# Kernel tuning notes

Measured on AMD Instinct MI355X. Metric: run time of the kernel, lower is better.

## Reference

```python
import jax, jax.numpy as jnp
import numpy as np


def setup_inputs() -> dict:
    key = jax.random.key(0)
    k = jax.random.split(key, 6)
    B = 65536
    x = jax.random.normal(k[0], (B, 784), dtype=jnp.float32)
    conv_w = jax.random.normal(k[1], (3, 3), dtype=jnp.float32)
    # torch Linear: weight [out,in], bias [out]; uniform(-1/sqrt(in),1/sqrt(in)) init approximated
    fc1_w = jax.random.uniform(k[2], (128, 26 * 26), dtype=jnp.float32, minval=-1, maxval=1) / jnp.sqrt(676.0)
    fc1_b = jax.random.uniform(k[3], (128,), dtype=jnp.float32, minval=-1, maxval=1) / jnp.sqrt(676.0)
    fc2_w = jax.random.uniform(k[4], (10, 128), dtype=jnp.float32, minval=-1, maxval=1) / jnp.sqrt(128.0)
    fc2_b = jax.random.uniform(k[5], (10,), dtype=jnp.float32, minval=-1, maxval=1) / jnp.sqrt(128.0)
    return {"x": x, "conv_w": conv_w, "fc1_w": fc1_w, "fc1_b": fc1_b, "fc2_w": fc2_w, "fc2_b": fc2_b}


def _forward(x, conv_w, fc1_w, fc1_b, fc2_w, fc2_b):
    B = x.shape[0]
    img = x.reshape(B, 1, 28, 28)  # NCHW, single channel
    kern = conv_w.reshape(1, 1, 3, 3)  # OIHW
    # valid 3x3 cross-correlation -> (B,1,26,26), same math as the nested-loop Convolve
    conv = jax.lax.conv_general_dilated(
        img, kern, window_strides=(1, 1), padding="VALID",
        dimension_numbers=("NCHW", "OIHW", "NCHW"))
    h = conv.reshape(B, 26 * 26)
    h = jax.nn.relu(h @ fc1_w.T + fc1_b)
    return h @ fc2_w.T + fc2_b  # (B,10)


def reference(x, conv_w, fc1_w, fc1_b, fc2_w, fc2_b):
    return _forward(x, conv_w, fc1_w, fc1_b, fc2_w, fc2_b)
```

## Files before the change

kernel.cpp:

```cpp
#include <hip/hip_runtime.h>
#include <hip/hip_bf16.h>

typedef float  f32x4  __attribute__((ext_vector_type(4)));
typedef short  short8 __attribute__((ext_vector_type(8)));

#define NKT   25
#define BM    64
#define AB    4096
#define BB    8192
#define BOFFS (3 * AB)
#define POOLB (3 * AB + 3 * BB)

static __device__ __forceinline__ unsigned short f2bf(float f) {
    unsigned int u = __float_as_uint(f);
    unsigned int r = (u + 0x7fffu + ((u >> 16) & 1u)) >> 16;
    return (unsigned short)r;
}
static __device__ __forceinline__ float bf2f(unsigned short h) {
    return __uint_as_float(((unsigned int)h) << 16);
}
static __device__ __forceinline__ uint2 pack4(f32x4 v) {
    __hip_bfloat162 p0 = __float22bfloat162_rn(make_float2(v[0], v[1]));
    __hip_bfloat162 p1 = __float22bfloat162_rn(make_float2(v[2], v[3]));
    uint2 r;
    r.x = *reinterpret_cast<unsigned int*>(&p0);
    r.y = *reinterpret_cast<unsigned int*>(&p1);
    return r;
}

__global__ __launch_bounds__(256) void weff_prep(
    const float* __restrict__ fc1_w,
    const float* __restrict__ conv_w,
    const float* __restrict__ fc2_w,
    unsigned short* __restrict__ ws)
{
    int idx = blockIdx.x * 256 + threadIdx.x;
    if (idx >= 128 * 800) return;
    if (idx < 1280) ws[102400 + idx] = f2bf(fc2_w[idx]);
    int o = idx / 800, p = idx - o * 800;
    float s = 0.f;
    if (p < 784) {
        int y = p / 28, xx = p - y * 28;
        #pragma unroll
        for (int dr = 0; dr < 3; ++dr) {
            int r = y - dr;
            if (r < 0 || r > 25) continue;
            #pragma unroll
            for (int dc = 0; dc < 3; ++dc) {
                int c = xx - dc;
                if (c < 0 || c > 25) continue;
                s += fc1_w[o * 676 + r * 26 + c] * conv_w[dr * 3 + dc];
            }
        }
    }
    int kt = p >> 5, kk = p & 31;
    ws[kt * 4096 + (kk >> 3) * 1024 + o * 8 + (kk & 7)] = f2bf(s);
}

__global__ __launch_bounds__(512, 8) void fused_fwd(
    const float* __restrict__ x,
    const unsigned short* __restrict__ weff4,
    const float* __restrict__ fc1_b,
    const float* __restrict__ fc2_b,
    float* __restrict__ out,
    int B)
{
    __shared__ __align__(16) char pool[POOLB];

    const int tid  = threadIdx.x;
    const int lane = tid & 63;
    const int wid  = tid >> 6;
    const int wr   = wid >> 1;
    const int wc   = wid & 1;
    const int r16  = lane & 15;
    const int kc   = lane >> 4;
    const int m0   = blockIdx.x * BM;
    const unsigned short* fc2wb = weff4 + 102400;

    const int sr = tid >> 3;
    const int g  = tid & 7;
    int grow = m0 + sr; if (grow >= B) grow = B - 1;
    const float* xr = x + (size_t)grow * 784;
    const int awb = (g >> 1) * 1024 + sr * 16 + (g & 1) * 8;

    f32x4 av[4];

#define LD_A(s_, kt_) do {                                                    \
        int k_ = (kt_) * 32 + g * 4; if (k_ > 780) k_ = 0;                    \
        av[s_] = *reinterpret_cast<const f32x4*>(xr + k_);                    \
    } while (0)

#define WR_A(s_, bi_) do {                                                    \
        uint2 q_ = pack4(av[s_]);                                             \
        *reinterpret_cast<uint2*>(pool + (bi_) * AB + awb) = q_;              \
    } while (0)

#define GL_B(bi_, kt_) __builtin_amdgcn_global_load_lds(                      \
        (const __attribute__((address_space(1))) void*)                      \
            (weff4 + (size_t)(kt_) * 4096 + tid * 8),                         \
        (__attribute__((address_space(3))) void*)                            \
            (pool + BOFFS + (bi_) * BB + tid * 16), 16, 0, 0)

    const int aoff = kc * 1024 + (wr * 16 + r16) * 16;
    const int boff = BOFFS + kc * 2048 + (wc * 64 + r16) * 16;

    f32x4 acc[4];
    #pragma unroll
    for (int j = 0; j < 4; ++j) acc[j] = (f32x4)(0.f);

    asm volatile("s_waitcnt vmcnt(0)" ::: "memory");

    GL_B(0, 0); GL_B(1, 1);
    LD_A(0, 0); LD_A(1, 1); LD_A(2, 2);
    WR_A(0, 0);

    #pragma unroll
    for (int i = 0; i < NKT; ++i) {
        asm volatile("s_waitcnt vmcnt(3) lgkmcnt(0)" ::: "memory");
        __builtin_amdgcn_s_barrier();
        __builtin_amdgcn_sched_barrier(0);

        const char* pa = pool + (i % 3) * AB;
        const char* pb = pool + (i % 3) * BB;
        short8 a0 = *reinterpret_cast<const short8*>(pa + aoff);
        short8 b0 = *reinterpret_cast<const short8*>(pb + boff);
        short8 b1 = *reinterpret_cast<const short8*>(pb + boff + 256);
        short8 b2 = *reinterpret_cast<const short8*>(pb + boff + 512);
        short8 b3 = *reinterpret_cast<const short8*>(pb + boff + 768);

        const int kb = (i + 2 <= 24) ? (i + 2) : 24;
        const int ka = (i + 3 <= 24) ? (i + 3) : 24;
        GL_B((i + 2) % 3, kb);
        LD_A((i + 3) % 4, ka);
        WR_A((i + 1) % 4, (i + 1) % 3);

        acc[0] = __builtin_amdgcn_mfma_f32_16x16x32_bf16(a0, b0, acc[0], 0, 0, 0);
        acc[1] = __builtin_amdgcn_mfma_f32_16x16x32_bf16(a0, b1, acc[1], 0, 0, 0);
        acc[2] = __builtin_amdgcn_mfma_f32_16x16x32_bf16(a0, b2, acc[2], 0, 0, 0);
        acc[3] = __builtin_amdgcn_mfma_f32_16x16x32_bf16(a0, b3, acc[3], 0, 0, 0);
    }
#undef LD_A
#undef WR_A
#undef GL_B

    asm volatile("s_waitcnt vmcnt(0) lgkmcnt(0)" ::: "memory");
    __builtin_amdgcn_s_barrier();
    __builtin_amdgcn_sched_barrier(0);

    unsigned short (*Hs)[136] = (unsigned short (*)[136])pool;
    #pragma unroll
    for (int j = 0; j < 4; ++j) {
        int ncol = wc * 64 + j * 16 + r16;
        float bias = fc1_b[ncol];
        #pragma unroll
        for (int r = 0; r < 4; ++r) {
            int mrow = wr * 16 + kc * 4 + r;
            float h = acc[j][r] + bias;
            Hs[mrow][ncol] = f2bf(h > 0.f ? h : 0.f);
        }
    }
    __syncthreads();

    #pragma unroll
    for (int it = 0; it < 2; ++it) {
        int idx = it * 512 + tid;
        if (idx < BM * 10) {
            int row = idx / 10, j = idx - row * 10;
            if ((m0 + row) < B) {
                float sum = fc2_b[j];
                const unsigned short* wrow = fc2wb + j * 128;
                #pragma unroll
                for (int n8 = 0; n8 < 16; ++n8) {
                    short8 h = *reinterpret_cast<const short8*>(&Hs[row][n8 * 8]);
                    short8 w = *reinterpret_cast<const short8*>(wrow + n8 * 8);
                    #pragma unroll
                    for (int k2 = 0; k2 < 8; ++k2)
                        sum += bf2f(((unsigned short*)&h)[k2]) *
                               bf2f(((unsigned short*)&w)[k2]);
                }
                out[(size_t)(m0 + row) * 10 + j] = sum;
            }
        }
    }
}

extern "C" void kernel_launch(void* const* d_in, const int* in_sizes, int n_in,
                              void* d_out, int out_size, void* d_ws, size_t ws_size,
                              hipStream_t stream) {
    const float* x      = (const float*)d_in[0];
    const float* conv_w = (const float*)d_in[1];
    const float* fc1_w  = (const float*)d_in[2];
    const float* fc1_b  = (const float*)d_in[3];
    const float* fc2_w  = (const float*)d_in[4];
    const float* fc2_b  = (const float*)d_in[5];
    float* out = (float*)d_out;
    unsigned short* ws = (unsigned short*)d_ws;

    int B = in_sizes[0] / 784;

    weff_prep<<<(128 * 800 + 255) / 256, 256, 0, stream>>>(fc1_w, conv_w, fc2_w, ws);

    int nblk = (B + BM - 1) / BM;
    fused_fwd<<<nblk, 512, 0, stream>>>(x, ws, fc1_b, fc2_b, out, B);
}
```

Measured before the change: 58.71 us.

## Double K-step per pipeline stage and handle the K tail separately

The main GEMM loop now consumes 64 K-elements per barrier-separated stage (two 32-wide weight tiles and wider A loads) instead of 32, cutting the iteration count from 25 to 12 and a separate tail step. The final 16-column tail of x is loaded directly into registers and multiplied against the last weight tile. This is meant to halve the barrier and wait overhead per K element and issue wider global loads. In exchange, shared memory per block doubles and the occupancy hint drops from 8 to 4 blocks, which may reduce latency hiding on this memory-bound kernel.

```diff
diff --git a/kernel.cpp b/kernel.cpp
--- a/kernel.cpp
+++ b/kernel.cpp
@@ -4,12 +4,12 @@
 typedef float  f32x4  __attribute__((ext_vector_type(4)));
 typedef short  short8 __attribute__((ext_vector_type(8)));
 
-#define NKT   25
+#define NMAIN 12
 #define BM    64
-#define AB    4096
-#define BB    8192
+#define AB    8192
+#define BBUF  16384
 #define BOFFS (3 * AB)
-#define POOLB (3 * AB + 3 * BB)
+#define POOLB (3 * AB + 3 * BBUF)
 
 static __device__ __forceinline__ unsigned short f2bf(float f) {
     unsigned int u = __float_as_uint(f);
@@ -57,9 +57,9 @@
     ws[kt * 4096 + (kk >> 3) * 1024 + o * 8 + (kk & 7)] = f2bf(s);
 }
 
-__global__ __launch_bounds__(512, 8) void fused_fwd(
+__global__ __launch_bounds__(512, 4) void fused_fwd(
     const float* __restrict__ x,
-    const unsigned short* __restrict__ weff4,
+    const unsigned short* __restrict__ weff,
     const float* __restrict__ fc1_b,
     const float* __restrict__ fc2_b,
     float* __restrict__ out,
@@ -75,34 +75,41 @@
     const int r16  = lane & 15;
     const int kc   = lane >> 4;
     const int m0   = blockIdx.x * BM;
-    const unsigned short* fc2wb = weff4 + 102400;
+    const unsigned short* fc2wb = weff + 102400;
 
     const int sr = tid >> 3;
     const int g  = tid & 7;
     int grow = m0 + sr; if (grow >= B) grow = B - 1;
     const float* xr = x + (size_t)grow * 784;
-    const int awb = (g >> 1) * 1024 + sr * 16 + (g & 1) * 8;
-
-    f32x4 av[4];
+    const int awb = (g >> 2) * 4096 + (g & 3) * 1024 + sr * 16;
+
+    f32x4 av[3][2];
 
 #define LD_A(s_, kt_) do {                                                    \
-        int k_ = (kt_) * 32 + g * 4; if (k_ > 780) k_ = 0;                    \
-        av[s_] = *reinterpret_cast<const f32x4*>(xr + k_);                    \
+        int k_ = (kt_) * 64 + g * 8; if (k_ > 776) k_ = 0;                    \
+        av[s_][0] = *reinterpret_cast<const f32x4*>(xr + k_);                 \
+        av[s_][1] = *reinterpret_cast<const f32x4*>(xr + k_ + 4);             \
     } while (0)
 
 #define WR_A(s_, bi_) do {                                                    \
-        uint2 q_ = pack4(av[s_]);                                             \
-        *reinterpret_cast<uint2*>(pool + (bi_) * AB + awb) = q_;              \
+        uint2 q0_ = pack4(av[s_][0]);                                         \
+        uint2 q1_ = pack4(av[s_][1]);                                         \
+        uint4 q_; q_.x = q0_.x; q_.y = q0_.y; q_.z = q1_.x; q_.w = q1_.y;     \
+        *reinterpret_cast<uint4*>(pool + (bi_) * AB + awb) = q_;              \
     } while (0)
 
-#define GL_B(bi_, kt_) __builtin_amdgcn_global_load_lds(                      \
+#define GL_B(bi_, tile_, h_) __builtin_amdgcn_global_load_lds(                \
         (const __attribute__((address_space(1))) void*)                      \
-            (weff4 + (size_t)(kt_) * 4096 + tid * 8),                         \
+            (weff + (size_t)(tile_) * 4096 + tid * 8),                        \
         (__attribute__((address_space(3))) void*)                            \
-            (pool + BOFFS + (bi_) * BB + tid * 16), 16, 0, 0)
-
-    const int aoff = kc * 1024 + (wr * 16 + r16) * 16;
-    const int boff = BOFFS + kc * 2048 + (wc * 64 + r16) * 16;
+            (pool + BOFFS + (bi_) * BBUF + (h_) * 8192 + tid * 16), 16, 0, 0)
+
+    const int arow = wr * 16 + r16;
+    const int aoff0 = 0    + kc * 1024 + arow * 16;
+    const int aoff1 = 4096 + kc * 1024 + arow * 16;
+    const int bcol = wc * 64 + r16;
+    const int boff0 = BOFFS + 0    + kc * 2048 + bcol * 16;
+    const int boff1 = BOFFS + 8192 + kc * 2048 + bcol * 16;
 
     f32x4 acc[4];
     #pragma unroll
@@ -110,40 +117,89 @@
 
     asm volatile("s_waitcnt vmcnt(0)" ::: "memory");
 
-    GL_B(0, 0); GL_B(1, 1);
-    LD_A(0, 0); LD_A(1, 1); LD_A(2, 2);
+    GL_B(0, 0, 0); GL_B(0, 1, 1);
+    GL_B(1, 2, 0); GL_B(1, 3, 1);
+    LD_A(0, 0); LD_A(1, 1);
     WR_A(0, 0);
 
     #pragma unroll
-    for (int i = 0; i < NKT; ++i) {
-        asm volatile("s_waitcnt vmcnt(3) lgkmcnt(0)" ::: "memory");
+    for (int i = 0; i < NMAIN; ++i) {
+        asm volatile("s_waitcnt vmcnt(4) lgkmcnt(0)" ::: "memory");
         __builtin_amdgcn_s_barrier();
         __builtin_amdgcn_sched_barrier(0);
 
         const char* pa = pool + (i % 3) * AB;
-        const char* pb = pool + (i % 3) * BB;
-        short8 a0 = *reinterpret_cast<const short8*>(pa + aoff);
-        short8 b0 = *reinterpret_cast<const short8*>(pb + boff);
-        short8 b1 = *reinterpret_cast<const short8*>(pb + boff + 256);
-        short8 b2 = *reinterpret_cast<const short8*>(pb + boff + 512);
-        short8 b3 = *reinterpret_cast<const short8*>(pb + boff + 768);
-
-        const int kb = (i + 2 <= 24) ? (i + 2) : 24;
-        const int ka = (i + 3 <= 24) ? (i + 3) : 24;
-        GL_B((i + 2) % 3, kb);
-        LD_A((i + 3) % 4, ka);
-        WR_A((i + 1) % 4, (i + 1) % 3);
-
-        acc[0] = __builtin_amdgcn_mfma_f32_16x16x32_bf16(a0, b0, acc[0], 0, 0, 0);
-        acc[1] = __builtin_amdgcn_mfma_f32_16x16x32_bf16(a0, b1, acc[1], 0, 0, 0);
-        acc[2] = __builtin_amdgcn_mfma_f32_16x16x32_bf16(a0, b2, acc[2], 0, 0, 0);
-        acc[3] = __builtin_amdgcn_mfma_f32_16x16x32_bf16(a0, b3, acc[3], 0, 0, 0);
+        const char* pb = pool + (i % 3) * BBUF;
+        short8 a0 = *reinterpret_cast<const short8*>(pa + aoff0);
+        short8 a1 = *reinterpret_cast<const short8*>(pa + aoff1);
+        short8 b00 = *reinterpret_cast<const short8*>(pb + boff0);
+        short8 b01 = *reinterpret_cast<const short8*>(pb + boff0 + 256);
+        short8 b02 = *reinterpret_cast<const short8*>(pb + boff0 + 512);
+        short8 b03 = *reinterpret_cast<const short8*>(pb + boff0 + 768);
+        short8 b10 = *reinterpret_cast<const short8*>(pb + boff1);
+        short8 b11 = *reinterpret_cast<const short8*>(pb + boff1 + 256);
+        short8 b12 = *reinterpret_cast<const short8*>(pb + boff1 + 512);
+        short8 b13 = *reinterpret_cast<const short8*>(pb + boff1 + 768);
+
+        const int t0 = (2 * (i + 2)     > 24) ? 24 : 2 * (i + 2);
+        const int t1 = (2 * (i + 2) + 1 > 24) ? 24 : 2 * (i + 2) + 1;
+        GL_B((i + 2) % 3, t0, 0);
+        GL_B((i + 2) % 3, t1, 1);
+        LD_A((i + 2) % 3, i + 2);
+        WR_A((i + 1) % 3, (i + 1) % 3);
+
+        acc[0] = __builtin_amdgcn_mfma_f32_16x16x32_bf16(a0, b00, acc[0], 0, 0, 0);
+        acc[1] = __builtin_amdgcn_mfma_f32_16x16x32_bf16(a0, b01, acc[1], 0, 0, 0);
+        acc[2] = __builtin_amdgcn_mfma_f32_16x16x32_bf16(a0, b02, acc[2], 0, 0, 0);
+        acc[3] = __builtin_amdgcn_mfma_f32_16x16x32_bf16(a0, b03, acc[3], 0, 0, 0);
+        acc[0] = __builtin_amdgcn_mfma_f32_16x16x32_bf16(a1, b10, acc[0], 0, 0, 0);
+        acc[1] = __builtin_amdgcn_mfma_f32_16x16x32_bf16(a1, b11, acc[1], 0, 0, 0);
+        acc[2] = __builtin_amdgcn_mfma_f32_16x16x32_bf16(a1, b12, acc[2], 0, 0, 0);
+        acc[3] = __builtin_amdgcn_mfma_f32_16x16x32_bf16(a1, b13, acc[3], 0, 0, 0);
     }
 #undef LD_A
 #undef WR_A
+
+    asm volatile("s_waitcnt vmcnt(0) lgkmcnt(0)" ::: "memory");
+    __builtin_amdgcn_s_barrier();
+    __builtin_amdgcn_sched_barrier(0);
+
+    GL_B(0, 24, 0);
+    f32x4 t0v = (f32x4)(0.f), t1v = (f32x4)(0.f);
+    {
+        int trow = m0 + wr * 16 + r16; if (trow >= B) trow = B - 1;
+        const float* xt = x + (size_t)trow * 784;
+        if (kc < 2) {
+            t0v = *reinterpret_cast<const f32x4*>(xt + 768 + kc * 8);
+            t1v = *reinterpret_cast<const f32x4*>(xt + 768 + kc * 8 + 4);
+        }
+    }
+    asm volatile("s_waitcnt vmcnt(0)" ::: "memory");
+    __builtin_amdgcn_s_barrier();
+    __builtin_amdgcn_sched_barrier(0);
+    {
+        __hip_bfloat162 p0 = __float22bfloat162_rn(make_float2(t0v[0], t0v[1]));
+        __hip_bfloat162 p1 = __float22bfloat162_rn(make_float2(t0v[2], t0v[3]));
+        __hip_bfloat162 p2 = __float22bfloat162_rn(make_float2(t1v[0], t1v[1]));
+        __hip_bfloat162 p3 = __float22bfloat162_rn(make_float2(t1v[2], t1v[3]));
+        short8 af;
+        reinterpret_cast<unsigned int*>(&af)[0] = *reinterpret_cast<unsigned int*>(&p0);
+        reinterpret_cast<unsigned int*>(&af)[1] = *reinterpret_cast<unsigned int*>(&p1);
+        reinterpret_cast<unsigned int*>(&af)[2] = *reinterpret_cast<unsigned int*>(&p2);
+        reinterpret_cast<unsigned int*>(&af)[3] = *reinterpret_cast<unsigned int*>(&p3);
+        const char* pb = pool;
+        short8 b0 = *reinterpret_cast<const short8*>(pb + boff0);
+        short8 b1 = *reinterpret_cast<const short8*>(pb + boff0 + 256);
+        short8 b2 = *reinterpret_cast<const short8*>(pb + boff0 + 512);
+        short8 b3 = *reinterpret_cast<const short8*>(pb + boff0 + 768);
+        acc[0] = __builtin_amdgcn_mfma_f32_16x16x32_bf16(af, b0, acc[0], 0, 0, 0);
+        acc[1] = __builtin_amdgcn_mfma_f32_16x16x32_bf16(af, b1, acc[1], 0, 0, 0);
+        acc[2] = __builtin_amdgcn_mfma_f32_16x16x32_bf16(af, b2, acc[2], 0, 0, 0);
+        acc[3] = __builtin_amdgcn_mfma_f32_16x16x32_bf16(af, b3, acc[3], 0, 0, 0);
+    }
 #undef GL_B
 
-    asm volatile("s_waitcnt vmcnt(0) lgkmcnt(0)" ::: "memory");
+    asm volatile("s_waitcnt lgkmcnt(0)" ::: "memory");
     __builtin_amdgcn_s_barrier();
     __builtin_amdgcn_sched_barrier(0);
 
```

Measured after the change: 61.75 us. 1.05x slower.

## Stage whole A tile in LDS upfront and stream B weights through registers

Applied to the files above, without the earlier changes.

Replaces the triple-buffered per-k-step LDS pipeline with a single bulk load of the block's full 64x784 input tile, converted to bf16 into padded LDS rows, followed by one barrier. The fc1 weights are now read directly from global/L2 into double-buffered registers instead of being copied into LDS with global_load_lds. This removes the per-iteration barriers and waitcnts, at the cost of about 100KB of LDS per block and lower occupancy (launch bounds changed from 8 to 2). Input loads are fully coalesced contiguous 32-byte chunks, but there is no overlap between the input load phase and the MFMA phase within a block.

```diff
diff --git a/kernel.cpp b/kernel.cpp
--- a/kernel.cpp
+++ b/kernel.cpp
@@ -4,12 +4,8 @@
 typedef float  f32x4  __attribute__((ext_vector_type(4)));
 typedef short  short8 __attribute__((ext_vector_type(8)));
 
-#define NKT   25
-#define BM    64
-#define AB    4096
-#define BB    8192
-#define BOFFS (3 * AB)
-#define POOLB (3 * AB + 3 * BB)
+#define BM 64
+#define RS 1600
 
 static __device__ __forceinline__ unsigned short f2bf(float f) {
     unsigned int u = __float_as_uint(f);
@@ -53,19 +49,18 @@
             }
         }
     }
-    int kt = p >> 5, kk = p & 31;
-    ws[kt * 4096 + (kk >> 3) * 1024 + o * 8 + (kk & 7)] = f2bf(s);
-}
-
-__global__ __launch_bounds__(512, 8) void fused_fwd(
+    ws[(p >> 5) * 4096 + ((p >> 3) & 3) * 1024 + o * 8 + (p & 7)] = f2bf(s);
+}
+
+__global__ __launch_bounds__(512, 2) void fused_fwd(
     const float* __restrict__ x,
-    const unsigned short* __restrict__ weff4,
+    const unsigned short* __restrict__ weff,
     const float* __restrict__ fc1_b,
     const float* __restrict__ fc2_b,
     float* __restrict__ out,
     int B)
 {
-    __shared__ __align__(16) char pool[POOLB];
+    __shared__ __align__(16) char pool[64 * RS];
 
     const int tid  = threadIdx.x;
     const int lane = tid & 63;
@@ -75,77 +70,85 @@
     const int r16  = lane & 15;
     const int kc   = lane >> 4;
     const int m0   = blockIdx.x * BM;
-    const unsigned short* fc2wb = weff4 + 102400;
-
-    const int sr = tid >> 3;
-    const int g  = tid & 7;
-    int grow = m0 + sr; if (grow >= B) grow = B - 1;
-    const float* xr = x + (size_t)grow * 784;
-    const int awb = (g >> 1) * 1024 + sr * 16 + (g & 1) * 8;
-
-    f32x4 av[4];
-
-#define LD_A(s_, kt_) do {                                                    \
-        int k_ = (kt_) * 32 + g * 4; if (k_ > 780) k_ = 0;                    \
-        av[s_] = *reinterpret_cast<const f32x4*>(xr + k_);                    \
+    const unsigned short* fc2wb = weff + 102400;
+
+    const float* xblk = x + (size_t)m0 * 784;
+
+    f32x4 av[8][2];
+#define LD_P(s_) do {                                                         \
+        const float* p_ = xblk + ((size_t)tid + 512 * (s_)) * 8;              \
+        av[(s_) & 7][0] = *reinterpret_cast<const f32x4*>(p_);                \
+        av[(s_) & 7][1] = *reinterpret_cast<const f32x4*>(p_ + 4);            \
     } while (0)
-
-#define WR_A(s_, bi_) do {                                                    \
-        uint2 q_ = pack4(av[s_]);                                             \
-        *reinterpret_cast<uint2*>(pool + (bi_) * AB + awb) = q_;              \
+#define WR_P(s_) do {                                                         \
+        int P_ = tid + 512 * (s_);                                            \
+        int row_ = P_ / 98, pr_ = P_ - row_ * 98;                             \
+        uint2 q0_ = pack4(av[(s_) & 7][0]);                                   \
+        uint2 q1_ = pack4(av[(s_) & 7][1]);                                   \
+        uint4 q_; q_.x = q0_.x; q_.y = q0_.y; q_.z = q1_.x; q_.w = q1_.y;     \
+        *reinterpret_cast<uint4*>(pool + row_ * RS + pr_ * 16) = q_;          \
     } while (0)
 
-#define GL_B(bi_, kt_) __builtin_amdgcn_global_load_lds(                      \
-        (const __attribute__((address_space(1))) void*)                      \
-            (weff4 + (size_t)(kt_) * 4096 + tid * 8),                         \
-        (__attribute__((address_space(3))) void*)                            \
-            (pool + BOFFS + (bi_) * BB + tid * 16), 16, 0, 0)
-
-    const int aoff = kc * 1024 + (wr * 16 + r16) * 16;
-    const int boff = BOFFS + kc * 2048 + (wc * 64 + r16) * 16;
+    LD_P(0); LD_P(1); LD_P(2); LD_P(3);
+    LD_P(4); LD_P(5); LD_P(6); LD_P(7);
+    WR_P(0); WR_P(1); WR_P(2); WR_P(3);
+    LD_P(8); LD_P(9); LD_P(10); LD_P(11);
+    WR_P(4); WR_P(5); WR_P(6); WR_P(7);
+
+    f32x4 tv0 = (f32x4)(0.f), tv1 = (f32x4)(0.f);
+    if (tid < 128) {
+        const float* p_ = xblk + ((size_t)6144 + tid) * 8;
+        tv0 = *reinterpret_cast<const f32x4*>(p_);
+        tv1 = *reinterpret_cast<const f32x4*>(p_ + 4);
+    }
+    WR_P(8); WR_P(9); WR_P(10); WR_P(11);
+    if (tid < 128) {
+        int P_ = 6144 + tid;
+        int row_ = P_ / 98, pr_ = P_ - row_ * 98;
+        uint2 q0_ = pack4(tv0), q1_ = pack4(tv1);
+        uint4 q_; q_.x = q0_.x; q_.y = q0_.y; q_.z = q1_.x; q_.w = q1_.y;
+        *reinterpret_cast<uint4*>(pool + row_ * RS + pr_ * 16) = q_;
+        int zr = tid >> 1, zp = 98 + (tid & 1);
+        uint4 z_; z_.x = 0; z_.y = 0; z_.z = 0; z_.w = 0;
+        *reinterpret_cast<uint4*>(pool + zr * RS + zp * 16) = z_;
+    }
+#undef LD_P
+#undef WR_P
+    __syncthreads();
+
+    const char* pa = pool + (wr * 16 + r16) * RS + kc * 16;
+    const unsigned short* wb = weff + kc * 1024 + (wc * 64 + r16) * 8;
+
+    short8 breg[2][4];
+#define LOADB(set_, kt_) do {                                                 \
+        const unsigned short* p_ = wb + (size_t)(kt_) * 4096;                 \
+        breg[set_][0] = *reinterpret_cast<const short8*>(p_);                 \
+        breg[set_][1] = *reinterpret_cast<const short8*>(p_ + 128);           \
+        breg[set_][2] = *reinterpret_cast<const short8*>(p_ + 256);           \
+        breg[set_][3] = *reinterpret_cast<const short8*>(p_ + 384);           \
+    } while (0)
 
     f32x4 acc[4];
     #pragma unroll
     for (int j = 0; j < 4; ++j) acc[j] = (f32x4)(0.f);
 
-    asm volatile("s_waitcnt vmcnt(0)" ::: "memory");
-
-    GL_B(0, 0); GL_B(1, 1);
-    LD_A(0, 0); LD_A(1, 1); LD_A(2, 2);
-    WR_A(0, 0);
-
-    #pragma unroll
-    for (int i = 0; i < NKT; ++i) {
-        asm volatile("s_waitcnt vmcnt(3) lgkmcnt(0)" ::: "memory");
-        __builtin_amdgcn_s_barrier();
-        __builtin_amdgcn_sched_barrier(0);
-
-        const char* pa = pool + (i % 3) * AB;
-        const char* pb = pool + (i % 3) * BB;
-        short8 a0 = *reinterpret_cast<const short8*>(pa + aoff);
-        short8 b0 = *reinterpret_cast<const short8*>(pb + boff);
-        short8 b1 = *reinterpret_cast<const short8*>(pb + boff + 256);
-        short8 b2 = *reinterpret_cast<const short8*>(pb + boff + 512);
-        short8 b3 = *reinterpret_cast<const short8*>(pb + boff + 768);
-
-        const int kb = (i + 2 <= 24) ? (i + 2) : 24;
-        const int ka = (i + 3 <= 24) ? (i + 3) : 24;
-        GL_B((i + 2) % 3, kb);
-        LD_A((i + 3) % 4, ka);
-        WR_A((i + 1) % 4, (i + 1) % 3);
-
-        acc[0] = __builtin_amdgcn_mfma_f32_16x16x32_bf16(a0, b0, acc[0], 0, 0, 0);
-        acc[1] = __builtin_amdgcn_mfma_f32_16x16x32_bf16(a0, b1, acc[1], 0, 0, 0);
-        acc[2] = __builtin_amdgcn_mfma_f32_16x16x32_bf16(a0, b2, acc[2], 0, 0, 0);
-        acc[3] = __builtin_amdgcn_mfma_f32_16x16x32_bf16(a0, b3, acc[3], 0, 0, 0);
-    }
-#undef LD_A
-#undef WR_A
-#undef GL_B
-
-    asm volatile("s_waitcnt vmcnt(0) lgkmcnt(0)" ::: "memory");
-    __builtin_amdgcn_s_barrier();
-    __builtin_amdgcn_sched_barrier(0);
+    LOADB(0, 0); LOADB(1, 1);
+
+    #pragma unroll
+    for (int kt = 0; kt < 25; ++kt) {
+        short8 a  = *reinterpret_cast<const short8*>(pa + kt * 64);
+        short8 b0 = breg[kt & 1][0], b1 = breg[kt & 1][1];
+        short8 b2 = breg[kt & 1][2], b3 = breg[kt & 1][3];
+        int kn = kt + 2; if (kn > 24) kn = 24;
+        LOADB(kt & 1, kn);
+        acc[0] = __builtin_amdgcn_mfma_f32_16x16x32_bf16(a, b0, acc[0], 0, 0, 0);
+        acc[1] = __builtin_amdgcn_mfma_f32_16x16x32_bf16(a, b1, acc[1], 0, 0, 0);
+        acc[2] = __builtin_amdgcn_mfma_f32_16x16x32_bf16(a, b2, acc[2], 0, 0, 0);
+        acc[3] = __builtin_amdgcn_mfma_f32_16x16x32_bf16(a, b3, acc[3], 0, 0, 0);
+    }
+#undef LOADB
+
+    __syncthreads();
 
     unsigned short (*Hs)[136] = (unsigned short (*)[136])pool;
     #pragma unroll
```

Result: slower. 82.03 us (+39.7%).
